# Performance work log

Hardware: AMD Instinct MI355X
Metric: run time of the kernel (lower is better)

Reference implementation:

```python
import jax, jax.numpy as jnp
import numpy as np

LN_EPS = 1e-5
SCALE = 2048 ** (-0.5)


def _layernorm(x):
    # LayerNorm over last dim, no affine params (elementwise_affine=False)
    mu = jnp.mean(x, axis=-1, keepdims=True)
    var = jnp.mean(jnp.square(x - mu), axis=-1, keepdims=True)
    return (x - mu) / jnp.sqrt(var + LN_EPS)


def setup_inputs() -> dict:
    key = jax.random.key(0)
    k1, k2, k3, k4 = jax.random.split(key, 4)
    B, N, M, D = 8, 2048, 2048, 2048
    x = jax.random.normal(k1, (B, N, D), dtype=jnp.float32)
    g = jax.random.normal(k2, (B, M, D), dtype=jnp.float32)
    # nn.Linear(dim, dim, bias=False) weights, shape [out, in]
    lim = 1.0 / np.sqrt(D)
    Wq = jax.random.uniform(k3, (D, D), dtype=jnp.float32, minval=-lim, maxval=lim)
    Wg = jax.random.uniform(k4, (D, D), dtype=jnp.float32, minval=-lim, maxval=lim)
    return {"x": x, "g": g, "Wq": Wq, "Wg": Wg}


def reference(x, g, Wq, Wg):
    # q = LN(x); rel_q = q @ Wq^T
    q = _layernorm(x)
    rel_q = jnp.einsum('bnd,ed->bne', q, Wq)
    # g = LN(g - mean_n(x)); rel_g = g @ Wg^T
    gc = _layernorm(g - jnp.mean(x, axis=1, keepdims=True))
    rel_g = jnp.einsum('bmd,ed->bme', gc, Wg)
    # scores [B, N, M], scaled softmax over M
    rel = jax.nn.softmax(jnp.einsum('bne,bme->bnm', rel_q, rel_g) * SCALE, axis=-1)
    # residual attention output
    return x + jnp.einsum('bnm,bmd->bnd', rel, gc)
```

## Files before the change

kernel.cpp:

```cpp
#include <hip/hip_runtime.h>
#include <hip/hip_bf16.h>
#include <stdint.h>

#define BB 8
#define NN 2048
#define MM 2048
#define DD 2048
#define LN_EPS 1e-5f
#define SM_SCALE 0.022097086912079608f

typedef __bf16 bf16_t;
typedef __attribute__((ext_vector_type(8))) __bf16 bf16x8;
typedef __attribute__((ext_vector_type(4))) float f32x4;

#define AS1(p) ((const __attribute__((address_space(1))) void*)(p))
#define AS3(p) ((__attribute__((address_space(3))) void*)(p))

__device__ __forceinline__ void wave_reduce2(float& a, float& b) {
#pragma unroll
  for (int off = 32; off > 0; off >>= 1) {
    a += __shfl_down(a, off, 64);
    b += __shfl_down(b, off, 64);
  }
}

__global__ __launch_bounds__(256) void colmean_kernel(const float* __restrict__ x,
                                                      float* __restrict__ xmean) {
  const int d = blockIdx.x * 256 + threadIdx.x;
  const int b = blockIdx.z;
  const int n0 = blockIdx.y * 128;
  const float* p = x + ((size_t)b * NN + n0) * DD + d;
  float s = 0.f;
#pragma unroll 8
  for (int i = 0; i < 128; ++i) s += p[(size_t)i * DD];
  atomicAdd(&xmean[b * DD + d], s * (1.0f / NN));
}

__global__ __launch_bounds__(256) void ln_x_kernel(const float* __restrict__ x,
                                                   bf16_t* __restrict__ out) {
  __shared__ float sa[4], sb[4];
  const size_t row = blockIdx.x;
  const float* xr = x + row * DD;
  const int tid = threadIdx.x;
  f32x4 v0 = *(const f32x4*)(xr + tid * 8);
  f32x4 v1 = *(const f32x4*)(xr + tid * 8 + 4);
  float s = 0.f, s2 = 0.f;
#pragma unroll
  for (int k = 0; k < 4; ++k) {
    s += v0[k] + v1[k];
    s2 += v0[k] * v0[k] + v1[k] * v1[k];
  }
  wave_reduce2(s, s2);
  const int wid = tid >> 6, lid = tid & 63;
  if (lid == 0) { sa[wid] = s; sb[wid] = s2; }
  __syncthreads();
  s = sa[0] + sa[1] + sa[2] + sa[3];
  s2 = sb[0] + sb[1] + sb[2] + sb[3];
  const float mu = s * (1.f / DD);
  const float var = s2 * (1.f / DD) - mu * mu;
  const float rstd = rsqrtf(var + LN_EPS);
  bf16x8 o;
#pragma unroll
  for (int k = 0; k < 4; ++k) {
    o[k] = (__bf16)((v0[k] - mu) * rstd);
    o[k + 4] = (__bf16)((v1[k] - mu) * rstd);
  }
  *(bf16x8*)(out + row * DD + tid * 8) = o;
}

__global__ __launch_bounds__(256) void ln_g_kernel(const float* __restrict__ g,
                                                   const float* __restrict__ xmean,
                                                   bf16_t* __restrict__ out) {
  __shared__ float sa[4], sb[4];
  const size_t row = blockIdx.x;
  const int b = (int)(row >> 11);
  const float* gr = g + row * DD;
  const float* xm = xmean + (size_t)b * DD;
  const int tid = threadIdx.x;
  f32x4 v0 = *(const f32x4*)(gr + tid * 8);
  f32x4 v1 = *(const f32x4*)(gr + tid * 8 + 4);
  f32x4 m0 = *(const f32x4*)(xm + tid * 8);
  f32x4 m1 = *(const f32x4*)(xm + tid * 8 + 4);
  float s = 0.f, s2 = 0.f;
#pragma unroll
  for (int k = 0; k < 4; ++k) {
    v0[k] -= m0[k];
    v1[k] -= m1[k];
    s += v0[k] + v1[k];
    s2 += v0[k] * v0[k] + v1[k] * v1[k];
  }
  wave_reduce2(s, s2);
  const int wid = tid >> 6, lid = tid & 63;
  if (lid == 0) { sa[wid] = s; sb[wid] = s2; }
  __syncthreads();
  s = sa[0] + sa[1] + sa[2] + sa[3];
  s2 = sb[0] + sb[1] + sb[2] + sb[3];
  const float mu = s * (1.f / DD);
  const float var = s2 * (1.f / DD) - mu * mu;
  const float rstd = rsqrtf(var + LN_EPS);
  bf16x8 o;
#pragma unroll
  for (int k = 0; k < 4; ++k) {
    o[k] = (__bf16)((v0[k] - mu) * rstd);
    o[k + 4] = (__bf16)((v1[k] - mu) * rstd);
  }
  *(bf16x8*)(out + row * DD + tid * 8) = o;
}

__global__ __launch_bounds__(256) void cvt_kernel(const float* __restrict__ in,
                                                  bf16_t* __restrict__ out, int n8) {
  const int i = blockIdx.x * 256 + threadIdx.x;
  if (i >= n8) return;
  f32x4 a = *(const f32x4*)(in + (size_t)i * 8);
  f32x4 b = *(const f32x4*)(in + (size_t)i * 8 + 4);
  bf16x8 o;
#pragma unroll
  for (int k = 0; k < 4; ++k) {
    o[k] = (__bf16)a[k];
    o[k + 4] = (__bf16)b[k];
  }
  *(bf16x8*)(out + (size_t)i * 8) = o;
}

__global__ __launch_bounds__(256) void transpose_kernel(const unsigned short* __restrict__ in,
                                                        unsigned short* __restrict__ out) {
  __shared__ unsigned short tile[32][33];
  const int b = blockIdx.z;
  const int m0 = blockIdx.y * 32, d0 = blockIdx.x * 32;
  const unsigned short* src = in + (size_t)b * MM * DD;
  unsigned short* dst = out + (size_t)b * DD * MM;
  const int tx = threadIdx.x, ty = threadIdx.y;
#pragma unroll
  for (int i = 0; i < 32; i += 8)
    tile[ty + i][tx] = src[(size_t)(m0 + ty + i) * DD + d0 + tx];
  __syncthreads();
#pragma unroll
  for (int i = 0; i < 32; i += 8)
    dst[(size_t)(d0 + ty + i) * MM + m0 + tx] = tile[tx][ty + i];
}

__global__ __launch_bounds__(256) void softmax_kernel(bf16_t* __restrict__ sc) {
  __shared__ float sh[4];
  const size_t row = blockIdx.x;
  bf16_t* pr = sc + row * MM;
  const int tid = threadIdx.x;
  const int wid = tid >> 6, lid = tid & 63;
  bf16x8 v = *(const bf16x8*)(pr + tid * 8);
  float f[8];
  float m = -1e30f;
#pragma unroll
  for (int k = 0; k < 8; ++k) {
    f[k] = (float)v[k];
    m = fmaxf(m, f[k]);
  }
#pragma unroll
  for (int off = 32; off > 0; off >>= 1) m = fmaxf(m, __shfl_down(m, off, 64));
  if (lid == 0) sh[wid] = m;
  __syncthreads();
  m = fmaxf(fmaxf(sh[0], sh[1]), fmaxf(sh[2], sh[3]));
  float s = 0.f;
#pragma unroll
  for (int k = 0; k < 8; ++k) {
    f[k] = __expf((f[k] - m) * SM_SCALE);
    s += f[k];
  }
  __syncthreads();
#pragma unroll
  for (int off = 32; off > 0; off >>= 1) s += __shfl_down(s, off, 64);
  if (lid == 0) sh[wid] = s;
  __syncthreads();
  s = sh[0] + sh[1] + sh[2] + sh[3];
  const float inv = 1.f / s;
  bf16x8 o;
#pragma unroll
  for (int k = 0; k < 8; ++k) o[k] = (__bf16)(f[k] * inv);
  *(bf16x8*)(pr + tid * 8) = o;
}

template <int MODE>
__global__ __launch_bounds__(512, 2) void gemm256_kernel(
    const bf16_t* __restrict__ A, const bf16_t* __restrict__ Bm,
    void* __restrict__ C, const float* __restrict__ resid,
    size_t sA, size_t sB) {
  extern __shared__ bf16_t lds[];
  const int tid = threadIdx.x;
  const int lane = tid & 63;
  const int wid = tid >> 6;
  const int wm = wid >> 2;
  const int wn = wid & 3;

  int bid = blockIdx.x;
  const int cpx = gridDim.x >> 3;
  bid = (bid & 7) * cpx + (bid >> 3);
  const int bz = bid >> 6;
  const int rem = bid & 63;
  const int m0 = (rem >> 3) << 8;
  const int n0 = (rem & 7) << 8;

  const bf16_t* Ab = A + (size_t)bz * sA;
  const bf16_t* Bb = Bm + (size_t)bz * sB;

  const int srow = tid >> 3;
  const int scol = ((tid & 7) ^ (srow & 7)) << 3;

  const int fr = lane & 15;
  const int kg = lane >> 4;
  const int swz = fr & 7;

  f32x4 acc[8][4] = {};

#define ISSUE_A(c, kt, o)                                                                  \
  __builtin_amdgcn_global_load_lds(                                                        \
      AS1(Ab + (size_t)(m0 + (o)*64 + srow) * 2048 + (kt)*64 + scol),                      \
      AS3(lds + (c)*32768 + (o)*4096 + tid * 8), 16, 0, 0)
#define ISSUE_B(c, kt, o)                                                                  \
  __builtin_amdgcn_global_load_lds(                                                        \
      AS1(Bb + (size_t)(n0 + (o)*64 + srow) * 2048 + (kt)*64 + scol),                      \
      AS3(lds + (c)*32768 + 16384 + (o)*4096 + tid * 8), 16, 0, 0)

  ISSUE_A(0, 0, 0); ISSUE_A(0, 0, 1); ISSUE_A(0, 0, 2); ISSUE_A(0, 0, 3);
  ISSUE_B(0, 0, 0); ISSUE_B(0, 0, 1); ISSUE_B(0, 0, 2); ISSUE_B(0, 0, 3);
  ISSUE_A(1, 1, 0); ISSUE_A(1, 1, 2);
  asm volatile("s_waitcnt vmcnt(2)" ::: "memory");
  __builtin_amdgcn_s_barrier();

  for (int t = 0; t < 32; ++t) {
    const int cur = t & 1;
    const int nxt = cur ^ 1;
    const bf16_t* Ar = lds + cur * 32768 + wm * 8192;
    const bf16_t* Br = lds + cur * 32768 + 16384 + (wn >> 1) * 8192 + (wn & 1) * 4096;
#pragma unroll
    for (int ph = 0; ph < 4; ++ph) {
      const int mh = ph >> 1, nh = ph & 1;
      bf16x8 af[4][2], bf[2][2];
#pragma unroll
      for (int i = 0; i < 4; ++i) {
        const int ra = (mh * 64 + i * 16 + fr) * 64;
#pragma unroll
        for (int ks = 0; ks < 2; ++ks)
          af[i][ks] = *(const bf16x8*)(Ar + ra + ((((ks << 2) + kg) ^ swz) << 3));
      }
#pragma unroll
      for (int j = 0; j < 2; ++j) {
        const int rb = (nh * 32 + j * 16 + fr) * 64;
#pragma unroll
        for (int ks = 0; ks < 2; ++ks)
          bf[j][ks] = *(const bf16x8*)(Br + rb + ((((ks << 2) + kg) ^ swz) << 3));
      }
      if (ph == 0 && t + 1 < 32) { ISSUE_A(nxt, t + 1, 1); ISSUE_A(nxt, t + 1, 3); }
      if (ph == 1 && t + 1 < 32) { ISSUE_B(nxt, t + 1, 0); ISSUE_B(nxt, t + 1, 1); }
      if (ph == 2 && t + 1 < 32) { ISSUE_B(nxt, t + 1, 2); ISSUE_B(nxt, t + 1, 3); }
      if (ph == 3 && t + 2 < 32) { ISSUE_A(cur, t + 2, 0); ISSUE_A(cur, t + 2, 2); }
      __builtin_amdgcn_s_barrier();
      __builtin_amdgcn_s_setprio(1);
#pragma unroll
      for (int i = 0; i < 4; ++i)
#pragma unroll
        for (int j = 0; j < 2; ++j)
#pragma unroll
          for (int ks = 0; ks < 2; ++ks)
            acc[mh * 4 + i][nh * 2 + j] = __builtin_amdgcn_mfma_f32_16x16x32_bf16(
                af[i][ks], bf[j][ks], acc[mh * 4 + i][nh * 2 + j], 0, 0, 0);
      __builtin_amdgcn_s_setprio(0);
      if (ph == 3) {
        if (t < 30) asm volatile("s_waitcnt vmcnt(2)" ::: "memory");
        else        asm volatile("s_waitcnt vmcnt(0)" ::: "memory");
      }
      __builtin_amdgcn_s_barrier();
    }
  }
#undef ISSUE_A
#undef ISSUE_B

  const int cr = kg << 2;
  const size_t cbase = (size_t)bz * 2048 * 2048;
#pragma unroll
  for (int mi = 0; mi < 8; ++mi) {
#pragma unroll
    for (int j = 0; j < 4; ++j) {
#pragma unroll
      for (int t4 = 0; t4 < 4; ++t4) {
        const int r = m0 + wm * 128 + mi * 16 + cr + t4;
        const int c = n0 + wn * 64 + j * 16 + fr;
        const size_t off = cbase + (size_t)r * 2048 + c;
        if (MODE == 0)
          ((bf16_t*)C)[off] = (__bf16)acc[mi][j][t4];
        else
          ((float*)C)[off] = resid[off] + acc[mi][j][t4];
      }
    }
  }
}

extern "C" void kernel_launch(void* const* d_in, const int* in_sizes, int n_in,
                              void* d_out, int out_size, void* d_ws, size_t ws_size,
                              hipStream_t stream) {
  const float* x = (const float*)d_in[0];
  const float* g = (const float*)d_in[1];
  const float* Wq = (const float*)d_in[2];
  const float* Wg = (const float*)d_in[3];
  float* out = (float*)d_out;

  uint8_t* ws = (uint8_t*)d_ws;
  const size_t SZ = (size_t)BB * NN * DD * 2;
  bf16_t* q_bf   = (bf16_t*)(ws + 0 * SZ);
  bf16_t* gc_bf  = (bf16_t*)(ws + 1 * SZ);
  bf16_t* gcT_bf = (bf16_t*)(ws + 2 * SZ);
  bf16_t* relq   = (bf16_t*)(ws + 3 * SZ);
  bf16_t* relg   = (bf16_t*)(ws + 4 * SZ);
  bf16_t* scores = (bf16_t*)(ws + 5 * SZ);
  bf16_t* Wq_bf  = (bf16_t*)(ws + 6 * SZ);
  bf16_t* Wg_bf  = (bf16_t*)(ws + 6 * SZ + (size_t)DD * DD * 2);
  float*  xmean  = (float*)(ws + 6 * SZ + (size_t)DD * DD * 4);

  const size_t TEN = (size_t)NN * DD;
  const int SMEM = 131072;
  hipFuncSetAttribute(reinterpret_cast<const void*>(gemm256_kernel<0>),
                      hipFuncAttributeMaxDynamicSharedMemorySize, SMEM);
  hipFuncSetAttribute(reinterpret_cast<const void*>(gemm256_kernel<1>),
                      hipFuncAttributeMaxDynamicSharedMemorySize, SMEM);

  hipMemsetAsync(xmean, 0, (size_t)BB * DD * sizeof(float), stream);

  const int n8 = DD * DD / 8;
  cvt_kernel<<<dim3((n8 + 255) / 256), dim3(256), 0, stream>>>(Wq, Wq_bf, n8);
  cvt_kernel<<<dim3((n8 + 255) / 256), dim3(256), 0, stream>>>(Wg, Wg_bf, n8);

  colmean_kernel<<<dim3(DD / 256, NN / 128, BB), dim3(256), 0, stream>>>(x, xmean);

  ln_x_kernel<<<dim3(BB * NN), dim3(256), 0, stream>>>(x, q_bf);
  ln_g_kernel<<<dim3(BB * MM), dim3(256), 0, stream>>>(g, xmean, gc_bf);

  transpose_kernel<<<dim3(DD / 32, MM / 32, BB), dim3(32, 8), 0, stream>>>(
      (const unsigned short*)gc_bf, (unsigned short*)gcT_bf);

  gemm256_kernel<0><<<dim3(512), dim3(512), SMEM, stream>>>(
      q_bf, Wq_bf, (void*)relq, nullptr, TEN, 0);
  gemm256_kernel<0><<<dim3(512), dim3(512), SMEM, stream>>>(
      gc_bf, Wg_bf, (void*)relg, nullptr, TEN, 0);

  gemm256_kernel<0><<<dim3(512), dim3(512), SMEM, stream>>>(
      relq, relg, (void*)scores, nullptr, TEN, TEN);

  softmax_kernel<<<dim3(BB * NN), dim3(256), 0, stream>>>(scores);

  gemm256_kernel<1><<<dim3(512), dim3(512), SMEM, stream>>>(
      scores, gcT_bf, (void*)out, x, TEN, TEN);
}
```

Measured before the change: 956.1 us.

## Restructure GEMM main loop into two-barrier half-step prefetch schedule

```diff
diff --git a/kernel.cpp b/kernel.cpp
--- a/kernel.cpp
+++ b/kernel.cpp
@@ -218,59 +218,79 @@
       AS1(Bb + (size_t)(n0 + (o)*64 + srow) * 2048 + (kt)*64 + scol),                      \
       AS3(lds + (c)*32768 + 16384 + (o)*4096 + tid * 8), 16, 0, 0)
 
-  ISSUE_A(0, 0, 0); ISSUE_A(0, 0, 1); ISSUE_A(0, 0, 2); ISSUE_A(0, 0, 3);
+#define READ_FRAGS(mh, nh)                                                                 \
+  {                                                                                        \
+    const bf16_t* Ar = lds + cur * 32768 + wm * 8192;                                      \
+    const bf16_t* Br = lds + cur * 32768 + 16384 + wn * 4096;                              \
+    _Pragma("unroll") for (int i = 0; i < 4; ++i) {                                        \
+      const int ra = ((mh)*64 + i * 16 + fr) * 64;                                         \
+      _Pragma("unroll") for (int ks = 0; ks < 2; ++ks)                                     \
+          af[i][ks] = *(const bf16x8*)(Ar + ra + ((((ks << 2) + kg) ^ swz) << 3));         \
+    }                                                                                      \
+    _Pragma("unroll") for (int j = 0; j < 2; ++j) {                                        \
+      const int rb = ((nh)*32 + j * 16 + fr) * 64;                                         \
+      _Pragma("unroll") for (int ks = 0; ks < 2; ++ks)                                     \
+          bf[j][ks] = *(const bf16x8*)(Br + rb + ((((ks << 2) + kg) ^ swz) << 3));         \
+    }                                                                                      \
+  }
+
+#define MFMA_BLOCK(mh, nh)                                                                 \
+  __builtin_amdgcn_s_setprio(1);                                                           \
+  _Pragma("unroll") for (int i = 0; i < 4; ++i)                                            \
+      _Pragma("unroll") for (int j = 0; j < 2; ++j)                                        \
+          _Pragma("unroll") for (int ks = 0; ks < 2; ++ks)                                 \
+              acc[(mh)*4 + i][(nh)*2 + j] = __builtin_amdgcn_mfma_f32_16x16x32_bf16(       \
+                  af[i][ks], bf[j][ks], acc[(mh)*4 + i][(nh)*2 + j], 0, 0, 0);             \
+  __builtin_amdgcn_s_setprio(0);
+
+#define WAITV(n) asm volatile("s_waitcnt vmcnt(" #n ")" ::: "memory")
+
+  ISSUE_A(0, 0, 0); ISSUE_A(0, 0, 2);
   ISSUE_B(0, 0, 0); ISSUE_B(0, 0, 1); ISSUE_B(0, 0, 2); ISSUE_B(0, 0, 3);
-  ISSUE_A(1, 1, 0); ISSUE_A(1, 1, 2);
-  asm volatile("s_waitcnt vmcnt(2)" ::: "memory");
+  ISSUE_A(0, 0, 1); ISSUE_A(0, 0, 3);
+  WAITV(2);
   __builtin_amdgcn_s_barrier();
 
-  for (int t = 0; t < 32; ++t) {
+  bf16x8 af[4][2], bf[2][2];
+
+  for (int t = 0; t < 31; ++t) {
     const int cur = t & 1;
     const int nxt = cur ^ 1;
-    const bf16_t* Ar = lds + cur * 32768 + wm * 8192;
-    const bf16_t* Br = lds + cur * 32768 + 16384 + (wn >> 1) * 8192 + (wn & 1) * 4096;
-#pragma unroll
-    for (int ph = 0; ph < 4; ++ph) {
-      const int mh = ph >> 1, nh = ph & 1;
-      bf16x8 af[4][2], bf[2][2];
-#pragma unroll
-      for (int i = 0; i < 4; ++i) {
-        const int ra = (mh * 64 + i * 16 + fr) * 64;
-#pragma unroll
-        for (int ks = 0; ks < 2; ++ks)
-          af[i][ks] = *(const bf16x8*)(Ar + ra + ((((ks << 2) + kg) ^ swz) << 3));
-      }
-#pragma unroll
-      for (int j = 0; j < 2; ++j) {
-        const int rb = (nh * 32 + j * 16 + fr) * 64;
-#pragma unroll
-        for (int ks = 0; ks < 2; ++ks)
-          bf[j][ks] = *(const bf16x8*)(Br + rb + ((((ks << 2) + kg) ^ swz) << 3));
-      }
-      if (ph == 0 && t + 1 < 32) { ISSUE_A(nxt, t + 1, 1); ISSUE_A(nxt, t + 1, 3); }
-      if (ph == 1 && t + 1 < 32) { ISSUE_B(nxt, t + 1, 0); ISSUE_B(nxt, t + 1, 1); }
-      if (ph == 2 && t + 1 < 32) { ISSUE_B(nxt, t + 1, 2); ISSUE_B(nxt, t + 1, 3); }
-      if (ph == 3 && t + 2 < 32) { ISSUE_A(cur, t + 2, 0); ISSUE_A(cur, t + 2, 2); }
-      __builtin_amdgcn_s_barrier();
-      __builtin_amdgcn_s_setprio(1);
-#pragma unroll
-      for (int i = 0; i < 4; ++i)
-#pragma unroll
-        for (int j = 0; j < 2; ++j)
-#pragma unroll
-          for (int ks = 0; ks < 2; ++ks)
-            acc[mh * 4 + i][nh * 2 + j] = __builtin_amdgcn_mfma_f32_16x16x32_bf16(
-                af[i][ks], bf[j][ks], acc[mh * 4 + i][nh * 2 + j], 0, 0, 0);
-      __builtin_amdgcn_s_setprio(0);
-      if (ph == 3) {
-        if (t < 30) asm volatile("s_waitcnt vmcnt(2)" ::: "memory");
-        else        asm volatile("s_waitcnt vmcnt(0)" ::: "memory");
-      }
-      __builtin_amdgcn_s_barrier();
-    }
+    READ_FRAGS(0, 0);
+    ISSUE_A(nxt, t + 1, 0); ISSUE_A(nxt, t + 1, 2);
+    ISSUE_B(nxt, t + 1, 0); ISSUE_B(nxt, t + 1, 1);
+    ISSUE_B(nxt, t + 1, 2); ISSUE_B(nxt, t + 1, 3);
+    MFMA_BLOCK(0, 0);
+    READ_FRAGS(0, 1);
+    MFMA_BLOCK(0, 1);
+    WAITV(6);
+    __builtin_amdgcn_s_barrier();
+    READ_FRAGS(1, 0);
+    ISSUE_A(nxt, t + 1, 1); ISSUE_A(nxt, t + 1, 3);
+    MFMA_BLOCK(1, 0);
+    READ_FRAGS(1, 1);
+    MFMA_BLOCK(1, 1);
+    WAITV(2);
+    __builtin_amdgcn_s_barrier();
+  }
+  {
+    const int cur = 1;
+    READ_FRAGS(0, 0);
+    MFMA_BLOCK(0, 0);
+    READ_FRAGS(0, 1);
+    MFMA_BLOCK(0, 1);
+    WAITV(0);
+    __builtin_amdgcn_s_barrier();
+    READ_FRAGS(1, 0);
+    MFMA_BLOCK(1, 0);
+    READ_FRAGS(1, 1);
+    MFMA_BLOCK(1, 1);
   }
 #undef ISSUE_A
 #undef ISSUE_B
+#undef READ_FRAGS
+#undef MFMA_BLOCK
+#undef WAITV
 
   const int cr = kg << 2;
   const size_t cbase = (size_t)bz * 2048 * 2048;
```

Measured after the change: 929.1 us. 2.8% less time.
